# Performance work log

Measured on AMD Instinct MI355X. Metric: run time of the kernel, lower is better.

## Reference

```python
import jax, jax.numpy as jnp
import numpy as np

SF = 2  # shrink_factor


def resize_bilinear_ac(x, oh, ow):
    """Bilinear resize with align_corners=True, NCHW, matches torch F.interpolate."""
    B, C, H, W = x.shape
    if (oh, ow) == (H, W):
        return x
    ys = jnp.linspace(0.0, H - 1, oh)
    y0 = jnp.floor(ys).astype(jnp.int32)
    y1 = jnp.clip(y0 + 1, 0, H - 1)
    wy = (ys - y0).astype(x.dtype)
    xs = jnp.linspace(0.0, W - 1, ow)
    x0 = jnp.floor(xs).astype(jnp.int32)
    x1 = jnp.clip(x0 + 1, 0, W - 1)
    wx = (xs - x0).astype(x.dtype)
    t = x[:, :, y0, :] * (1 - wy)[None, None, :, None] + x[:, :, y1, :] * wy[None, None, :, None]
    return t[:, :, :, x0] * (1 - wx) + t[:, :, :, x1] * wx


def conv1x1(x, W, b):
    # x: [B,C,H,W], W: [O,C], b: [O]
    return jnp.einsum('bchw,oc->bohw', x, W) + b[None, :, None, None]


def setup_inputs() -> dict:
    key = jax.random.key(0)
    ks = jax.random.split(key, 8)
    B, C, H, W = 4, 512, 129, 129
    Cqk = C // 8
    s = 1.0 / np.sqrt(C)
    return {
        'x': jax.random.normal(ks[0], (B, C, H, W), jnp.float32),
        'Wq': jax.random.normal(ks[1], (Cqk, C), jnp.float32) * s,
        'bq': jax.random.normal(ks[2], (Cqk,), jnp.float32) * s,
        'Wk': jax.random.normal(ks[3], (Cqk, C), jnp.float32) * s,
        'bk': jax.random.normal(ks[4], (Cqk,), jnp.float32) * s,
        'Wv': jax.random.normal(ks[5], (C, C), jnp.float32) * s,
        'bv': jax.random.normal(ks[6], (C,), jnp.float32) * s,
        'gamma': jax.random.normal(ks[7], (1,), jnp.float32) * 0.1,
    }


def reference(x, Wq, bq, Wk, bk, Wv, bv, gamma):
    B, C, H, W = x.shape
    h = (H - 1) // SF + 1
    w = (W - 1) // SF + 1
    xs = resize_bilinear_ac(x, h, w)  # [B,C,h,w]
    N = h * w
    q = conv1x1(xs, Wq, bq).reshape(B, -1, N)  # [B,Cqk,N]
    k = conv1x1(xs, Wk, bk).reshape(B, -1, N)  # [B,Cqk,N]
    v = conv1x1(xs, Wv, bv).reshape(B, -1, N)  # [B,C,N]
    # energy[b,n,m] = <q[:,n], k[:,m]>
    energy = jnp.einsum('bcn,bcm->bnm', q, k)  # [B,N,N]
    attention = jax.nn.softmax(energy, axis=-1)
    # out[b,c,n] = sum_m v[b,c,m] * attention[b,n,m]  (bmm(value, attention^T))
    out = jnp.einsum('bcm,bnm->bcn', v, attention).reshape(B, C, h, w)
    Hu = (h - 1) * SF + 1
    Wu = (w - 1) * SF + 1
    out = resize_bilinear_ac(out, Hu, Wu)
    out = gamma[0] * out + x
    return out, energy
```

## Files before the change

### kernel.cpp

```cpp
#include <hip/hip_runtime.h>
#include <hip/hip_bf16.h>
#include <cstdint>

#define BB 4
#define CC 512
#define CQK 64
#define HH 129
#define WW 129
#define HS 65
#define WSZ 65
#define NN 4225
#define NP 4352
#define KPV 4288
#define OUTSZ 34080768
#define ESZ 17850625

typedef unsigned short u16;
typedef __attribute__((ext_vector_type(8))) __bf16 bfrag;
typedef __attribute__((ext_vector_type(4))) float f4v;

__device__ inline u16 f2bf(float f) {
    union { float f; unsigned int u; } v; v.f = f;
    unsigned int u = v.u;
    return (u16)((u + 0x7FFFu + ((u >> 16) & 1u)) >> 16);
}
__device__ inline float bf2f(u16 v) {
    union { unsigned u; float f; } x; x.u = (unsigned)v << 16; return x.f;
}

__device__ __forceinline__ void gload16(const u16* g, u16* l) {
    __builtin_amdgcn_global_load_lds(
        (const __attribute__((address_space(1))) void*)g,
        (__attribute__((address_space(3))) void*)l, 16, 0, 0);
}

__global__ __launch_bounds__(256) void cast_weights(const float* __restrict__ Wq,
                                                    const float* __restrict__ Wk,
                                                    const float* __restrict__ Wv,
                                                    u16* __restrict__ Wc) {
    int idx = blockIdx.x * 256 + threadIdx.x;
    if (idx >= 640 * 512) return;
    int o = idx >> 9, c = idx & 511;
    float v = (o < 64) ? Wq[o * 512 + c] : (o < 128) ? Wk[(o - 64) * 512 + c] : Wv[(o - 128) * 512 + c];
    Wc[idx] = f2bf(v);
}

__global__ __launch_bounds__(256) void subsample_t(const float* __restrict__ x, u16* __restrict__ XsT) {
    __shared__ u16 tile[64][65];
    int nt = blockIdx.x, ct = blockIdx.y, b = blockIdx.z;
    int t = threadIdx.x;
#pragma unroll
    for (int l = 0; l < 16; ++l) {
        int e = t + l * 256;
        int ci = e >> 6, nj = e & 63;
        int n = nt * 64 + nj;
        int nc = n < (NN - 1) ? n : (NN - 1);
        int i = nc / 65, j = nc % 65;
        int c = ct * 64 + ci;
        float v = x[(((size_t)b * CC + c) * HH + 2 * i) * WW + 2 * j];
        tile[ci][nj] = f2bf(v);
    }
    __syncthreads();
#pragma unroll
    for (int l = 0; l < 16; ++l) {
        int e = t + l * 256;
        int nj = e >> 6, ci = e & 63;
        XsT[((size_t)b * NP + nt * 64 + nj) * 512 + ct * 64 + ci] = tile[ci][nj];
    }
}

template <int MODE>
__global__ __launch_bounds__(256) void gemm_nt(const u16* __restrict__ Abase,
                                               const u16* __restrict__ Bbase,
                                               int K, int lda, int ldb,
                                               float* __restrict__ outF,
                                               u16* __restrict__ out1, u16* __restrict__ out2,
                                               const float* __restrict__ bq,
                                               const float* __restrict__ bk,
                                               const float* __restrict__ bv,
                                               float* __restrict__ psums) {
    __shared__ __align__(16) u16 S[16384];
    u16* As = S;
    u16* Bs = S + 8192;

    const int z = blockIdx.z;
    const u16* A; const u16* Bm;
    if (MODE == 0) { A = Abase;                          Bm = Bbase + (size_t)z * NP * 512; }
    if (MODE == 1) { A = Abase + (size_t)z * NP * 128;   Bm = Bbase + (size_t)z * NP * 128 + 64; }

    const size_t m0 = (size_t)blockIdx.y * 128;
    const size_t n0 = (size_t)blockIdx.x * 128;
    const u16* Ab = A + m0 * lda;
    const u16* Bb = Bm + n0 * ldb;

    const int tid = threadIdx.x;
    const int lane = tid & 63, w = tid >> 6;
    const int wr = w >> 1, wc = w & 1;
    const int frow = lane & 15, fk = (lane >> 4) * 8;

    f4v acc[4][4];
#pragma unroll
    for (int i = 0; i < 4; ++i)
#pragma unroll
        for (int j = 0; j < 4; ++j) acc[i][j] = (f4v){0.f, 0.f, 0.f, 0.f};

    for (int kt = 0; kt < K; kt += 64) {
        if (kt) __syncthreads();
#pragma unroll
        for (int it = 0; it < 4; ++it) {
            int cb = (it * 4 + w) * 64;
            int chunk = cb + lane;
            int r = chunk >> 3;
            int kc = (chunk & 7) << 3;
            gload16(Ab + (size_t)r * lda + kt + kc, &As[cb * 8]);
            gload16(Bb + (size_t)r * ldb + kt + kc, &Bs[cb * 8]);
        }
        __syncthreads();
#pragma unroll
        for (int ks = 0; ks < 2; ++ks) {
            bfrag af[4], bf[4];
#pragma unroll
            for (int i = 0; i < 4; ++i)
                af[i] = *(const bfrag*)&As[(wr * 64 + i * 16 + frow) * 64 + ks * 32 + fk];
#pragma unroll
            for (int j = 0; j < 4; ++j)
                bf[j] = *(const bfrag*)&Bs[(wc * 64 + j * 16 + frow) * 64 + ks * 32 + fk];
#pragma unroll
            for (int i = 0; i < 4; ++i)
#pragma unroll
                for (int j = 0; j < 4; ++j)
                    acc[i][j] = __builtin_amdgcn_mfma_f32_16x16x32_bf16(af[i], bf[j], acc[i][j], 0, 0, 0);
        }
    }

    const int rbase = (lane >> 4) * 4, cbase = lane & 15;

    if (MODE == 0) {
        u16* out1b = out1 + (size_t)z * NP * 128;
        u16* out2b = out2 + (size_t)z * 512 * NP;
#pragma unroll
        for (int i = 0; i < 4; ++i)
#pragma unroll
            for (int j = 0; j < 4; ++j) {
                size_t row0 = m0 + wr * 64 + i * 16 + rbase;
                size_t col = n0 + wc * 64 + j * 16 + cbase;
#pragma unroll
                for (int r = 0; r < 4; ++r) {
                    int o = (int)(row0 + r);
                    float bias = (o < 64) ? bq[o] : (o < 128) ? bk[o - 64] : bv[o - 128];
                    u16 bb = f2bf(acc[i][j][r] + bias);
                    if (o < 128) out1b[col * 128 + o] = bb;
                    else out2b[(size_t)(o - 128) * NP + col] = bb;
                }
            }
    } else {
        float* eb = outF + (size_t)z * ESZ;
        u16* Pb = out1 + (size_t)z * NP * NP;
        float psl[4][4];
#pragma unroll
        for (int i = 0; i < 4; ++i)
#pragma unroll
            for (int r = 0; r < 4; ++r) psl[i][r] = 0.f;

        __syncthreads();
#pragma unroll
        for (int i = 0; i < 4; ++i)
#pragma unroll
            for (int j = 0; j < 4; ++j) {
                int rl = wr * 64 + i * 16 + rbase;
                int cl = wc * 64 + j * 16 + cbase;
                size_t row0 = m0 + rl;
                size_t col = n0 + cl;
#pragma unroll
                for (int r = 0; r < 4; ++r) {
                    float v = acc[i][j][r];
                    size_t ro = row0 + r;
                    float pe = (col < NN) ? __expf(v) : 0.f;
                    if (ro < NN && col < NN) eb[ro * NN + col] = v;
                    S[(rl + r) * 128 + cl] = f2bf(pe);
                    psl[i][r] += pe;
                }
            }
        float* pbase = psums + ((size_t)z * 68 + blockIdx.x * 2 + wc) * NP;
#pragma unroll
        for (int i = 0; i < 4; ++i)
#pragma unroll
            for (int r = 0; r < 4; ++r) {
                float s = psl[i][r];
                s += __shfl_xor(s, 1);
                s += __shfl_xor(s, 2);
                s += __shfl_xor(s, 4);
                s += __shfl_xor(s, 8);
                if (cbase == 0)
                    pbase[m0 + wr * 64 + i * 16 + rbase + r] = s;
            }
        __syncthreads();
        u16* pb = Pb + m0 * NP + n0;
#pragma unroll
        for (int l = 0; l < 8; ++l) {
            int idx = tid + l * 256;
            int row = idx >> 4, c16 = idx & 15;
            *(int4*)(pb + (size_t)row * NP + c16 * 8) = *(const int4*)&S[row * 128 + c16 * 8];
        }
    }
}

__global__ __launch_bounds__(256) void reduce_sums(const float* __restrict__ psums,
                                                   float* __restrict__ invsum) {
    int idx = blockIdx.x * 256 + threadIdx.x;
    if (idx >= BB * NP) return;
    int b = idx / NP, n = idx % NP;
    const float* p = psums + (size_t)b * 68 * NP + n;
    float s = 0.f;
#pragma unroll
    for (int ct = 0; ct < 68; ++ct) s += p[(size_t)ct * NP];
    invsum[idx] = 1.f / s;
}

__global__ __launch_bounds__(256) void gemm_pv(const u16* __restrict__ Vb,
                                               const u16* __restrict__ P,
                                               u16* __restrict__ ctxp,
                                               const float* __restrict__ invsum) {
    __shared__ __align__(16) u16 S[16384];
    u16* As = S;
    u16* Bs = S + 8192;

    unsigned flat = blockIdx.x + 34u * (blockIdx.y + 4u * blockIdx.z);
    unsigned swz = (flat & 7u) * 136u + (flat >> 3);
    unsigned zs = swz / 136u;
    unsigned rem = swz - zs * 136u;
    unsigned xs = rem >> 2;
    unsigned ys = rem & 3u;
    const int b = (int)(zs >> 1), half = (int)(zs & 1);

    const u16* A = Vb + (size_t)b * 512 * NP;
    const u16* Bm = P + (size_t)b * NP * NP;
    const size_t m0 = (size_t)ys * 128;
    const size_t n0 = (size_t)xs * 128;
    const u16* Ab = A + m0 * NP;
    const u16* Bb = Bm + n0 * NP;
    const int kbeg = half ? 2176 : 0;
    const int kend = half ? KPV : 2176;

    const int tid = threadIdx.x;
    const int lane = tid & 63, w = tid >> 6;
    const int wr = w >> 1, wc = w & 1;
    const int frow = lane & 15, fk = (lane >> 4) * 8;

    f4v acc[4][4];
#pragma unroll
    for (int i = 0; i < 4; ++i)
#pragma unroll
        for (int j = 0; j < 4; ++j) acc[i][j] = (f4v){0.f, 0.f, 0.f, 0.f};

    for (int kt = kbeg; kt < kend; kt += 64) {
        if (kt != kbeg) __syncthreads();
#pragma unroll
        for (int it = 0; it < 4; ++it) {
            int cb = (it * 4 + w) * 64;
            int chunk = cb + lane;
            int r = chunk >> 3;
            int kc = (chunk & 7) << 3;
            gload16(Ab + (size_t)r * NP + kt + kc, &As[cb * 8]);
            gload16(Bb + (size_t)r * NP + kt + kc, &Bs[cb * 8]);
        }
        __syncthreads();
#pragma unroll
        for (int ks = 0; ks < 2; ++ks) {
            bfrag af[4], bf[4];
#pragma unroll
            for (int i = 0; i < 4; ++i)
                af[i] = *(const bfrag*)&As[(wr * 64 + i * 16 + frow) * 64 + ks * 32 + fk];
#pragma unroll
            for (int j = 0; j < 4; ++j)
                bf[j] = *(const bfrag*)&Bs[(wc * 64 + j * 16 + frow) * 64 + ks * 32 + fk];
#pragma unroll
            for (int i = 0; i < 4; ++i)
#pragma unroll
                for (int j = 0; j < 4; ++j)
                    acc[i][j] = __builtin_amdgcn_mfma_f32_16x16x32_bf16(af[i], bf[j], acc[i][j], 0, 0, 0);
        }
    }

    const int rbase = (lane >> 4) * 4, cbase = lane & 15;
    const float* isb = invsum + (size_t)b * NP;
    __syncthreads();
#pragma unroll
    for (int j = 0; j < 4; ++j) {
        int cl = wc * 64 + j * 16 + cbase;
        float inv = isb[n0 + cl];
#pragma unroll
        for (int i = 0; i < 4; ++i) {
            int rl = wr * 64 + i * 16 + rbase;
#pragma unroll
            for (int r = 0; r < 4; ++r)
                S[(rl + r) * 128 + cl] = f2bf(acc[i][j][r] * inv);
        }
    }
    __syncthreads();
    u16* cb = ctxp + ((size_t)(half * BB + b) * 512 + m0) * NP + n0;
#pragma unroll
    for (int l = 0; l < 8; ++l) {
        int idx = tid + l * 256;
        int row = idx >> 4, c16 = idx & 15;
        *(int4*)(cb + (size_t)row * NP + c16 * 8) = *(const int4*)&S[row * 128 + c16 * 8];
    }
}

#define SLICE ((size_t)BB * 512 * NP)
__global__ __launch_bounds__(256) void upsample_add(const u16* __restrict__ ctxp,
                                                    const float* __restrict__ x,
                                                    const float* __restrict__ gm,
                                                    float* __restrict__ out) {
    unsigned q = blockIdx.x * 256 + threadIdx.x;
    if (q >= (OUTSZ / 4)) return;
    unsigned idx0 = q * 4;
    float g = gm[0];
    float4 xv = *(const float4*)&x[idx0];
    float ov[4];
#pragma unroll
    for (int e = 0; e < 4; ++e) {
        unsigned idx = idx0 + e;
        unsigned xx = idx % WW;
        unsigned t = idx / WW;
        unsigned yy = t % HH;
        unsigned bc = t / HH;
        const u16* cb = ctxp + (size_t)bc * NP;
        unsigned i0 = yy >> 1, j0 = xx >> 1;
        unsigned n00 = i0 * 65 + j0;
        float wy = 0.5f * (float)(yy & 1), wx = 0.5f * (float)(xx & 1);
        float c00 = 0.f, c01 = 0.f, c10 = 0.f, c11 = 0.f;
#pragma unroll
        for (int sl = 0; sl < 2; ++sl) {
            const u16* p = cb + (size_t)sl * SLICE;
            c00 += bf2f(p[n00]);
            c01 += bf2f(p[n00 + 1]);
            c10 += bf2f(p[n00 + 65]);
            c11 += bf2f(p[n00 + 66]);
        }
        float cx0 = c00 + wx * (c01 - c00);
        float cx1 = c10 + wx * (c11 - c10);
        ov[e] = g * (cx0 + wy * (cx1 - cx0));
    }
    float4 o4 = {ov[0] + xv.x, ov[1] + xv.y, ov[2] + xv.z, ov[3] + xv.w};
    *(float4*)&out[idx0] = o4;
}

#define SZ_WC    ((size_t)640 * 512 * 2)
#define OFF_XST  (SZ_WC)
#define SZ_XST   ((size_t)BB * NP * 512 * 2)
#define OFF_QKT  (OFF_XST + SZ_XST)
#define SZ_QKT   ((size_t)BB * NP * 128 * 2)
#define OFF_V    (OFF_QKT + SZ_QKT)
#define SZ_V     ((size_t)BB * 512 * NP * 2)
#define OFF_PS   (OFF_V + SZ_V)
#define SZ_PS    ((size_t)BB * 68 * NP * 4)
#define OFF_INV  (OFF_PS + SZ_PS)
#define SZ_INV   ((size_t)BB * NP * 4)
#define OFF_CTXP (OFF_INV + SZ_INV)
#define SZ_CTXP  ((size_t)2 * BB * 512 * NP * 2)
#define OFF_P    (OFF_CTXP + SZ_CTXP)

extern "C" void kernel_launch(void* const* d_in, const int* in_sizes, int n_in,
                              void* d_out, int out_size, void* d_ws, size_t ws_size,
                              hipStream_t stream) {
    const float* x  = (const float*)d_in[0];
    const float* Wq = (const float*)d_in[1];
    const float* bq = (const float*)d_in[2];
    const float* Wk = (const float*)d_in[3];
    const float* bk = (const float*)d_in[4];
    const float* Wv = (const float*)d_in[5];
    const float* bv = (const float*)d_in[6];
    const float* gm = (const float*)d_in[7];

    float* out = (float*)d_out;
    float* energy = out + (size_t)OUTSZ;

    char* ws = (char*)d_ws;
    u16* Wc    = (u16*)(ws);
    u16* XsT   = (u16*)(ws + OFF_XST);
    u16* qkT   = (u16*)(ws + OFF_QKT);
    u16* V     = (u16*)(ws + OFF_V);
    float* psums  = (float*)(ws + OFF_PS);
    float* invsum = (float*)(ws + OFF_INV);
    u16* ctxp  = (u16*)(ws + OFF_CTXP);
    u16* P     = (u16*)(ws + OFF_P);

    cast_weights<<<1280, 256, 0, stream>>>(Wq, Wk, Wv, Wc);
    subsample_t<<<dim3(68, 8, BB), 256, 0, stream>>>(x, XsT);
    gemm_nt<0><<<dim3(34, 5, BB), 256, 0, stream>>>(Wc, XsT, 512, 512, 512,
                                                    nullptr, qkT, V, bq, bk, bv, nullptr);
    gemm_nt<1><<<dim3(34, 34, BB), 256, 0, stream>>>(qkT, qkT, 64, 128, 128,
                                                     energy, P, nullptr, nullptr, nullptr, nullptr,
                                                     psums);
    reduce_sums<<<68, 256, 0, stream>>>(psums, invsum);
    gemm_pv<<<dim3(34, 4, 8), 256, 0, stream>>>(V, P, ctxp, invsum);
    upsample_add<<<(OUTSZ / 4 + 255) / 256, 256, 0, stream>>>(ctxp, x, gm, out);
}
```

Before: 460.8 us.

## Merge setup kernels, remap projection GEMM grid, stage upsample planes in LDS

Merges weight casting and subsampling into one launch, saving a kernel launch. Flattens the projection GEMM grid and reorders it so blocks are grouped by batch and N-half, which may improve L2 locality. Rewrites upsample_add so each block handles one channel plane: it first sums the two context slices into shared memory, then interpolates from LDS. This removes the repeated global gathers and per-element division by 129*129, but the output writes become scalar instead of float4 and each plane is limited to 256 threads.

```diff
diff --git a/kernel.cpp b/kernel.cpp
--- a/kernel.cpp
+++ b/kernel.cpp
@@ -14,6 +14,7 @@
 #define KPV 4288
 #define OUTSZ 34080768
 #define ESZ 17850625
+#define PLANE 16641
 
 typedef unsigned short u16;
 typedef __attribute__((ext_vector_type(8))) __bf16 bfrag;
@@ -34,20 +35,24 @@
         (__attribute__((address_space(3))) void*)l, 16, 0, 0);
 }
 
-__global__ __launch_bounds__(256) void cast_weights(const float* __restrict__ Wq,
-                                                    const float* __restrict__ Wk,
-                                                    const float* __restrict__ Wv,
-                                                    u16* __restrict__ Wc) {
-    int idx = blockIdx.x * 256 + threadIdx.x;
-    if (idx >= 640 * 512) return;
-    int o = idx >> 9, c = idx & 511;
-    float v = (o < 64) ? Wq[o * 512 + c] : (o < 128) ? Wk[(o - 64) * 512 + c] : Wv[(o - 128) * 512 + c];
-    Wc[idx] = f2bf(v);
-}
-
-__global__ __launch_bounds__(256) void subsample_t(const float* __restrict__ x, u16* __restrict__ XsT) {
+__global__ __launch_bounds__(256) void setup_k(const float* __restrict__ Wq,
+                                               const float* __restrict__ Wk,
+                                               const float* __restrict__ Wv,
+                                               const float* __restrict__ x,
+                                               u16* __restrict__ Wc,
+                                               u16* __restrict__ XsT) {
     __shared__ u16 tile[64][65];
-    int nt = blockIdx.x, ct = blockIdx.y, b = blockIdx.z;
+    if (blockIdx.x < 1280) {
+        int idx = blockIdx.x * 256 + threadIdx.x;
+        int o = idx >> 9, c = idx & 511;
+        float v = (o < 64) ? Wq[o * 512 + c] : (o < 128) ? Wk[(o - 64) * 512 + c] : Wv[(o - 128) * 512 + c];
+        Wc[idx] = f2bf(v);
+        return;
+    }
+    int bid = blockIdx.x - 1280;
+    int nt = bid % 68;
+    int ct = (bid / 68) & 7;
+    int b = bid / 544;
     int t = threadIdx.x;
 #pragma unroll
     for (int l = 0; l < 16; ++l) {
@@ -83,13 +88,27 @@
     u16* As = S;
     u16* Bs = S + 8192;
 
-    const int z = blockIdx.z;
+    int z; size_t m0, n0; unsigned xsave = 0;
+    if (MODE == 0) {
+        unsigned flat = blockIdx.x;
+        unsigned s = flat & 7u;
+        unsigned k = flat >> 3;
+        unsigned m = k % 5u;
+        unsigned nl = k / 5u;
+        z = (int)(s >> 1);
+        m0 = (size_t)m * 128;
+        n0 = ((size_t)(s & 1u) * 17u + nl) * 128;
+    } else {
+        z = blockIdx.z;
+        m0 = (size_t)blockIdx.y * 128;
+        n0 = (size_t)blockIdx.x * 128;
+        xsave = blockIdx.x;
+    }
+
     const u16* A; const u16* Bm;
     if (MODE == 0) { A = Abase;                          Bm = Bbase + (size_t)z * NP * 512; }
     if (MODE == 1) { A = Abase + (size_t)z * NP * 128;   Bm = Bbase + (size_t)z * NP * 128 + 64; }
 
-    const size_t m0 = (size_t)blockIdx.y * 128;
-    const size_t n0 = (size_t)blockIdx.x * 128;
     const u16* Ab = A + m0 * lda;
     const u16* Bb = Bm + n0 * ldb;
 
@@ -181,7 +200,7 @@
                     psl[i][r] += pe;
                 }
             }
-        float* pbase = psums + ((size_t)z * 68 + blockIdx.x * 2 + wc) * NP;
+        float* pbase = psums + ((size_t)z * 68 + xsave * 2 + wc) * NP;
 #pragma unroll
         for (int i = 0; i < 4; ++i)
 #pragma unroll
@@ -312,38 +331,33 @@
                                                     const float* __restrict__ x,
                                                     const float* __restrict__ gm,
                                                     float* __restrict__ out) {
-    unsigned q = blockIdx.x * 256 + threadIdx.x;
-    if (q >= (OUTSZ / 4)) return;
-    unsigned idx0 = q * 4;
-    float g = gm[0];
-    float4 xv = *(const float4*)&x[idx0];
-    float ov[4];
-#pragma unroll
-    for (int e = 0; e < 4; ++e) {
-        unsigned idx = idx0 + e;
-        unsigned xx = idx % WW;
-        unsigned t = idx / WW;
-        unsigned yy = t % HH;
-        unsigned bc = t / HH;
-        const u16* cb = ctxp + (size_t)bc * NP;
-        unsigned i0 = yy >> 1, j0 = xx >> 1;
-        unsigned n00 = i0 * 65 + j0;
+    __shared__ float cs[66 * 66];
+    const int bc = blockIdx.x;
+    const u16* p0 = ctxp + (size_t)bc * NP;
+    const u16* p1 = p0 + SLICE;
+    const int t = threadIdx.x;
+
+    for (int idx = t; idx < 4225; idx += 256) {
+        int r = idx / 65, c = idx - r * 65;
+        cs[r * 66 + c] = bf2f(p0[idx]) + bf2f(p1[idx]);
+    }
+    if (t < 66) cs[t * 66 + 65] = 0.f;
+    if (t >= 128 && t < 193) cs[65 * 66 + (t - 128)] = 0.f;
+    __syncthreads();
+
+    const float g = gm[0];
+    const float* xb = x + (size_t)bc * PLANE;
+    float* ob = out + (size_t)bc * PLANE;
+    for (int idx = t; idx < PLANE; idx += 256) {
+        int yy = idx / 129, xx = idx - yy * 129;
+        int i0 = yy >> 1, j0 = xx >> 1;
         float wy = 0.5f * (float)(yy & 1), wx = 0.5f * (float)(xx & 1);
-        float c00 = 0.f, c01 = 0.f, c10 = 0.f, c11 = 0.f;
-#pragma unroll
-        for (int sl = 0; sl < 2; ++sl) {
-            const u16* p = cb + (size_t)sl * SLICE;
-            c00 += bf2f(p[n00]);
-            c01 += bf2f(p[n00 + 1]);
-            c10 += bf2f(p[n00 + 65]);
-            c11 += bf2f(p[n00 + 66]);
-        }
+        const float* c0 = &cs[i0 * 66 + j0];
+        float c00 = c0[0], c01 = c0[1], c10 = c0[66], c11 = c0[67];
         float cx0 = c00 + wx * (c01 - c00);
         float cx1 = c10 + wx * (c11 - c10);
-        ov[e] = g * (cx0 + wy * (cx1 - cx0));
-    }
-    float4 o4 = {ov[0] + xv.x, ov[1] + xv.y, ov[2] + xv.z, ov[3] + xv.w};
-    *(float4*)&out[idx0] = o4;
+        ob[idx] = g * (cx0 + wy * (cx1 - cx0)) + xb[idx];
+    }
 }
 
 #define SZ_WC    ((size_t)640 * 512 * 2)
@@ -386,14 +400,13 @@
     u16* ctxp  = (u16*)(ws + OFF_CTXP);
     u16* P     = (u16*)(ws + OFF_P);
 
-    cast_weights<<<1280, 256, 0, stream>>>(Wq, Wk, Wv, Wc);
-    subsample_t<<<dim3(68, 8, BB), 256, 0, stream>>>(x, XsT);
-    gemm_nt<0><<<dim3(34, 5, BB), 256, 0, stream>>>(Wc, XsT, 512, 512, 512,
-                                                    nullptr, qkT, V, bq, bk, bv, nullptr);
+    setup_k<<<3456, 256, 0, stream>>>(Wq, Wk, Wv, x, Wc, XsT);
+    gemm_nt<0><<<680, 256, 0, stream>>>(Wc, XsT, 512, 512, 512,
+                                        nullptr, qkT, V, bq, bk, bv, nullptr);
     gemm_nt<1><<<dim3(34, 34, BB), 256, 0, stream>>>(qkT, qkT, 64, 128, 128,
                                                      energy, P, nullptr, nullptr, nullptr, nullptr,
                                                      psums);
     reduce_sums<<<68, 256, 0, stream>>>(psums, invsum);
     gemm_pv<<<dim3(34, 4, 8), 256, 0, stream>>>(V, P, ctxp, invsum);
-    upsample_add<<<(OUTSZ / 4 + 255) / 256, 256, 0, stream>>>(ctxp, x, gm, out);
-}
+    upsample_add<<<2048, 256, 0, stream>>>(ctxp, x, gm, out);
+}
```

Measured after the change: 420.3 us (median of 3 runs). 8.8% less time.
